# Kernel tuning notes

Measured on AMD Instinct MI355X. Metric: run time of the kernel, lower is better.

Reference implementation:

```python
import jax, jax.numpy as jnp
import numpy as np

LAMB_LABELS = 1.0
LAMB_BBOXES = 5.0
LAMB_GENIOU = 2.0


def box_cxcywh_to_xyxy(x):
    cx, cy, w, h = x[..., 0], x[..., 1], x[..., 2], x[..., 3]
    return jnp.stack([cx - 0.5 * w, cy - 0.5 * h, cx + 0.5 * w, cy + 0.5 * h], axis=-1)


def generalized_box_iou(b1, b2):
    # b1: [P,4] xyxy, b2: [T,4] xyxy -> [P,T] pairwise GIoU
    area1 = (b1[:, 2] - b1[:, 0]) * (b1[:, 3] - b1[:, 1])
    area2 = (b2[:, 2] - b2[:, 0]) * (b2[:, 3] - b2[:, 1])
    lt = jnp.maximum(b1[:, None, :2], b2[None, :, :2])
    rb = jnp.minimum(b1[:, None, 2:], b2[None, :, 2:])
    wh = jnp.clip(rb - lt, 0.0)
    inter = wh[..., 0] * wh[..., 1]
    union = area1[:, None] + area2[None, :] - inter
    iou = inter / union
    lt_e = jnp.minimum(b1[:, None, :2], b2[None, :, :2])
    rb_e = jnp.maximum(b1[:, None, 2:], b2[None, :, 2:])
    wh_e = jnp.clip(rb_e - lt_e, 0.0)
    area_e = wh_e[..., 0] * wh_e[..., 1]
    return iou - (area_e - union) / area_e


def setup_inputs() -> dict:
    key = jax.random.key(0)
    k1, k2, k3, k4 = jax.random.split(key, 4)
    B, N, C, T = 16, 900, 92, 960
    out_labels = jax.random.normal(k1, (B, N, C), dtype=jnp.float32)
    out_bboxes = jax.random.uniform(k2, (B, N, 4), dtype=jnp.float32)
    tgt_labels = jax.random.randint(k3, (T,), 0, C, dtype=jnp.int64)
    tgt_bboxes = jax.random.uniform(k4, (T, 4), dtype=jnp.float32)
    return {"out_labels": out_labels, "out_bboxes": out_bboxes,
            "tgt_labels": tgt_labels, "tgt_bboxes": tgt_bboxes}


def reference(out_labels, out_bboxes, tgt_labels, tgt_bboxes):
    B, N, C = out_labels.shape
    # '(b n) d' softmax over classes, then gather target-label columns
    probs = jax.nn.softmax(out_labels.reshape(B * N, C), axis=-1)
    cost_labels = 1.0 - probs[:, tgt_labels]                     # [BN, T]
    ob = out_bboxes.reshape(B * N, 4)
    # pairwise L1 (torch.cdist p=1)
    cost_bboxes = jnp.sum(jnp.abs(ob[:, None, :] - tgt_bboxes[None, :, :]), axis=-1)
    # NOTE: original converts only predicted boxes to xyxy (targets used as-is)
    cost_geniou = 1.0 - generalized_box_iou(box_cxcywh_to_xyxy(ob), tgt_bboxes)
    cost = (LAMB_LABELS * cost_labels + LAMB_BBOXES * cost_bboxes
            + LAMB_GENIOU * cost_geniou)
    return cost.reshape(B, N, -1)                                # [B, N, T]
```

## Files before the change

### kernel.cpp

```cpp
#include <hip/hip_runtime.h>
#include <math.h>

constexpr int kC = 92, kT = 960;
constexpr int kBN = 14400;
constexpr int WPB = 4;
constexpr int THREADS = WPB * 64;

typedef float vf2 __attribute__((ext_vector_type(2)));

__global__ __launch_bounds__(THREADS, 8) void matcher_kernel(
    const float* __restrict__ out_labels,
    const float* __restrict__ out_bboxes,
    const int*   __restrict__ tgt_labels,
    const float* __restrict__ tgt_bboxes,
    float*       __restrict__ cost)
{
    __shared__ float2 s_cl2[WPB][96];

    const int tid  = threadIdx.x;
    const int w    = tid >> 6;
    const int lane = tid & 63;
    const int p0   = (blockIdx.x * WPB + w) * 2;

    const float* lr0 = out_labels + (size_t)p0 * kC;
    const float* lr1 = lr0 + kC;
    float e00 = __expf(lr0[lane]);
    float e10 = __expf(lr1[lane]);
    float e01 = (lane + 64 < kC) ? __expf(lr0[lane + 64]) : 0.0f;
    float e11 = (lane + 64 < kC) ? __expf(lr1[lane + 64]) : 0.0f;
    float s0 = e00 + e01, s1 = e10 + e11;
    #pragma unroll
    for (int m = 1; m < 64; m <<= 1) {
        s0 += __shfl_xor(s0, m, 64);
        s1 += __shfl_xor(s1, m, 64);
    }
    float inv0 = __builtin_amdgcn_rcpf(s0);
    float inv1 = __builtin_amdgcn_rcpf(s1);
    s_cl2[w][lane] = make_float2(fmaf(-e00, inv0, 5.0f), fmaf(-e10, inv1, 5.0f));
    if (lane + 64 < kC)
        s_cl2[w][lane + 64] =
            make_float2(fmaf(-e01, inv0, 5.0f), fmaf(-e11, inv1, 5.0f));

    float4 bbA = ((const float4*)out_bboxes)[p0];
    float4 bbB = ((const float4*)out_bboxes)[p0 + 1];
    vf2 bcA = {bbA.x, bbA.y}, whA = {bbA.z, bbA.w};
    vf2 bcB = {bbB.x, bbB.y}, whB = {bbB.z, bbB.w};
    vf2 hA = whA * 0.5f,  hB = whB * 0.5f;
    vf2 b0A = bcA - hA,   b1A = bcA + hA;
    vf2 b0B = bcB - hB,   b1B = bcB + hB;
    float area1A = (b1A.x - b0A.x) * (b1A.y - b0A.y);
    float area1B = (b1B.x - b0B.x) * (b1B.y - b0B.y);

    asm volatile("s_waitcnt lgkmcnt(0)" ::: "memory");

    const float4* tb4 = (const float4*)tgt_bboxes;
    float* crow0 = cost + (size_t)p0 * kT;
    float* crow1 = crow0 + kT;

    auto row_cost = [&](vf2 b0, vf2 b1, vf2 bc, vf2 wh, float area1,
                        vf2 t0, vf2 t1, vf2 wt, float a2, float cls) -> float {
        vf2 lt = {fmaxf(b0.x, t0.x), fmaxf(b0.y, t0.y)};
        vf2 rb = {fminf(b1.x, t1.x), fminf(b1.y, t1.y)};
        vf2 iwu = rb - lt;
        float iw = fmaxf(iwu.x, 0.0f), ih = fmaxf(iwu.y, 0.0f);
        float inter = iw * ih;
        vf2 ew = (wh + wt) - iwu;
        float area_e = ew.x * ew.y;
        float uni = (area1 + a2) - inter;
        vf2 d0 = bc - t0, d1 = wh - t1;
        float l1 = fabsf(d0.x) + fabsf(d0.y) + fabsf(d1.x) + fabsf(d1.y);
        float num = fmaf(uni, uni, inter * area_e);
        float rcp = __builtin_amdgcn_rcpf(uni * area_e);
        float v = fmaf(5.0f, l1, cls);
        return fmaf(-2.0f * num, rcp, v);
    };

    #pragma unroll 5
    for (int k = 0; k < 15; ++k) {
        const int t = lane + 64 * k;
        float4 tbb = tb4[t];
        int    lb  = tgt_labels[t];
        float2 cls = s_cl2[w][lb];
        vf2 t0 = {tbb.x, tbb.y}, t1 = {tbb.z, tbb.w};
        vf2 wt = t1 - t0;
        float a2 = wt.x * wt.y;
        crow0[t] = row_cost(b0A, b1A, bcA, whA, area1A, t0, t1, wt, a2, cls.x);
        crow1[t] = row_cost(b0B, b1B, bcB, whB, area1B, t0, t1, wt, a2, cls.y);
    }
}

extern "C" void kernel_launch(void* const* d_in, const int* in_sizes, int n_in,
                              void* d_out, int out_size, void* d_ws, size_t ws_size,
                              hipStream_t stream) {
    const float* out_labels = (const float*)d_in[0];
    const float* out_bboxes = (const float*)d_in[1];
    const int*   tgt_labels = (const int*)d_in[2];
    const float* tgt_bboxes = (const float*)d_in[3];
    float* cost = (float*)d_out;
    dim3 grid(kBN / (WPB * 2));
    matcher_kernel<<<grid, THREADS, 0, stream>>>(out_labels, out_bboxes,
                                                 tgt_labels, tgt_bboxes, cost);
}
```

Before: 88.65 us.

## Process four prediction rows per wave and two targets per lane with vectorized stores

Each wave now handles four prediction rows instead of two, so every target box and label load is reused across four rows, and the class-cost table is stored as a float4 per class. Each lane processes two adjacent targets per iteration and writes float2 stores, with a 64-target tail loop. The grid halves, launch bounds drop to 4 blocks per CU, and register pressure rises. The kernel is dominated by output writes, so the gain is limited to fewer loads and wider stores.

After: 88.39 us, median of 2. Within noise of the previous version (-0.3%).

```diff
diff --git a/kernel.cpp b/kernel.cpp
--- a/kernel.cpp
+++ b/kernel.cpp
@@ -5,69 +5,68 @@
 constexpr int kBN = 14400;
 constexpr int WPB = 4;
 constexpr int THREADS = WPB * 64;
+constexpr int RPW = 4;
 
 typedef float vf2 __attribute__((ext_vector_type(2)));
 
-__global__ __launch_bounds__(THREADS, 8) void matcher_kernel(
+__global__ __launch_bounds__(THREADS, 4) void matcher_kernel(
     const float* __restrict__ out_labels,
     const float* __restrict__ out_bboxes,
     const int*   __restrict__ tgt_labels,
     const float* __restrict__ tgt_bboxes,
     float*       __restrict__ cost)
 {
-    __shared__ float2 s_cl2[WPB][96];
+    __shared__ float s_cl[WPB][96][4];
 
     const int tid  = threadIdx.x;
     const int w    = tid >> 6;
     const int lane = tid & 63;
-    const int p0   = (blockIdx.x * WPB + w) * 2;
+    const int p0   = (blockIdx.x * WPB + w) * RPW;
 
-    const float* lr0 = out_labels + (size_t)p0 * kC;
-    const float* lr1 = lr0 + kC;
-    float e00 = __expf(lr0[lane]);
-    float e10 = __expf(lr1[lane]);
-    float e01 = (lane + 64 < kC) ? __expf(lr0[lane + 64]) : 0.0f;
-    float e11 = (lane + 64 < kC) ? __expf(lr1[lane + 64]) : 0.0f;
-    float s0 = e00 + e01, s1 = e10 + e11;
+    const float* lr = out_labels + (size_t)p0 * kC;
+    float e0[RPW], e1[RPW], s[RPW];
+    #pragma unroll
+    for (int r = 0; r < RPW; ++r) {
+        e0[r] = __expf(lr[r * kC + lane]);
+        e1[r] = (lane + 64 < kC) ? __expf(lr[r * kC + lane + 64]) : 0.0f;
+        s[r] = e0[r] + e1[r];
+    }
     #pragma unroll
     for (int m = 1; m < 64; m <<= 1) {
-        s0 += __shfl_xor(s0, m, 64);
-        s1 += __shfl_xor(s1, m, 64);
+        #pragma unroll
+        for (int r = 0; r < RPW; ++r)
+            s[r] += __shfl_xor(s[r], m, 64);
     }
-    float inv0 = __builtin_amdgcn_rcpf(s0);
-    float inv1 = __builtin_amdgcn_rcpf(s1);
-    s_cl2[w][lane] = make_float2(fmaf(-e00, inv0, 5.0f), fmaf(-e10, inv1, 5.0f));
-    if (lane + 64 < kC)
-        s_cl2[w][lane + 64] =
-            make_float2(fmaf(-e01, inv0, 5.0f), fmaf(-e11, inv1, 5.0f));
+    #pragma unroll
+    for (int r = 0; r < RPW; ++r) {
+        float inv = __builtin_amdgcn_rcpf(s[r]);
+        s_cl[w][lane][r] = fmaf(-e0[r], inv, 5.0f);
+        if (lane + 64 < kC) s_cl[w][lane + 64][r] = fmaf(-e1[r], inv, 5.0f);
+    }
 
-    float4 bbA = ((const float4*)out_bboxes)[p0];
-    float4 bbB = ((const float4*)out_bboxes)[p0 + 1];
-    vf2 bcA = {bbA.x, bbA.y}, whA = {bbA.z, bbA.w};
-    vf2 bcB = {bbB.x, bbB.y}, whB = {bbB.z, bbB.w};
-    vf2 hA = whA * 0.5f,  hB = whB * 0.5f;
-    vf2 b0A = bcA - hA,   b1A = bcA + hA;
-    vf2 b0B = bcB - hB,   b1B = bcB + hB;
-    float area1A = (b1A.x - b0A.x) * (b1A.y - b0A.y);
-    float area1B = (b1B.x - b0B.x) * (b1B.y - b0B.y);
+    vf2 bc[RPW], wh[RPW], b0[RPW], b1[RPW]; float area1[RPW];
+    #pragma unroll
+    for (int r = 0; r < RPW; ++r) {
+        float4 bb = ((const float4*)out_bboxes)[p0 + r];
+        bc[r] = vf2{bb.x, bb.y}; wh[r] = vf2{bb.z, bb.w};
+        vf2 h = wh[r] * 0.5f;
+        b0[r] = bc[r] - h; b1[r] = bc[r] + h;
+        area1[r] = (b1[r].x - b0[r].x) * (b1[r].y - b0[r].y);
+    }
 
     asm volatile("s_waitcnt lgkmcnt(0)" ::: "memory");
 
-    const float4* tb4 = (const float4*)tgt_bboxes;
-    float* crow0 = cost + (size_t)p0 * kT;
-    float* crow1 = crow0 + kT;
-
-    auto row_cost = [&](vf2 b0, vf2 b1, vf2 bc, vf2 wh, float area1,
-                        vf2 t0, vf2 t1, vf2 wt, float a2, float cls) -> float {
-        vf2 lt = {fmaxf(b0.x, t0.x), fmaxf(b0.y, t0.y)};
-        vf2 rb = {fminf(b1.x, t1.x), fminf(b1.y, t1.y)};
+    auto row_cost = [&](int r, vf2 t0, vf2 t1, vf2 wt, float a2,
+                        float cls) -> float {
+        vf2 lt = {fmaxf(b0[r].x, t0.x), fmaxf(b0[r].y, t0.y)};
+        vf2 rb = {fminf(b1[r].x, t1.x), fminf(b1[r].y, t1.y)};
         vf2 iwu = rb - lt;
         float iw = fmaxf(iwu.x, 0.0f), ih = fmaxf(iwu.y, 0.0f);
         float inter = iw * ih;
-        vf2 ew = (wh + wt) - iwu;
+        vf2 ew = (wh[r] + wt) - iwu;
         float area_e = ew.x * ew.y;
-        float uni = (area1 + a2) - inter;
-        vf2 d0 = bc - t0, d1 = wh - t1;
+        float uni = (area1[r] + a2) - inter;
+        vf2 d0 = bc[r] - t0, d1 = wh[r] - t1;
         float l1 = fabsf(d0.x) + fabsf(d0.y) + fabsf(d1.x) + fabsf(d1.y);
         float num = fmaf(uni, uni, inter * area_e);
         float rcp = __builtin_amdgcn_rcpf(uni * area_e);
@@ -75,17 +74,43 @@
         return fmaf(-2.0f * num, rcp, v);
     };
 
-    #pragma unroll 5
-    for (int k = 0; k < 15; ++k) {
-        const int t = lane + 64 * k;
-        float4 tbb = tb4[t];
-        int    lb  = tgt_labels[t];
-        float2 cls = s_cl2[w][lb];
-        vf2 t0 = {tbb.x, tbb.y}, t1 = {tbb.z, tbb.w};
-        vf2 wt = t1 - t0;
-        float a2 = wt.x * wt.y;
-        crow0[t] = row_cost(b0A, b1A, bcA, whA, area1A, t0, t1, wt, a2, cls.x);
-        crow1[t] = row_cost(b0B, b1B, bcB, whB, area1B, t0, t1, wt, a2, cls.y);
+    const float4* tb4 = (const float4*)tgt_bboxes;
+    float* crow = cost + (size_t)p0 * kT;
+
+    #pragma unroll 2
+    for (int k = 0; k < 7; ++k) {
+        const int tA = lane * 2 + 128 * k;
+        float4 fa = tb4[tA];
+        float4 fb = tb4[tA + 1];
+        int2 lb = ((const int2*)tgt_labels)[lane + 64 * k];
+        float4 clsA = *(const float4*)s_cl[w][lb.x];
+        float4 clsB = *(const float4*)s_cl[w][lb.y];
+        vf2 ta0 = {fa.x, fa.y}, ta1 = {fa.z, fa.w};
+        vf2 tb0 = {fb.x, fb.y}, tb1 = {fb.z, fb.w};
+        vf2 wtA = ta1 - ta0, wtB = tb1 - tb0;
+        float a2A = wtA.x * wtA.y, a2B = wtB.x * wtB.y;
+        const float cA[4] = {clsA.x, clsA.y, clsA.z, clsA.w};
+        const float cB[4] = {clsB.x, clsB.y, clsB.z, clsB.w};
+        #pragma unroll
+        for (int r = 0; r < RPW; ++r) {
+            vf2 out;
+            out[0] = row_cost(r, ta0, ta1, wtA, a2A, cA[r]);
+            out[1] = row_cost(r, tb0, tb1, wtB, a2B, cB[r]);
+            *(vf2*)(crow + r * kT + tA) = out;
+        }
+    }
+
+    {
+        const int t = 896 + lane;
+        float4 ft = tb4[t];
+        int lb = tgt_labels[t];
+        float4 cls = *(const float4*)s_cl[w][lb];
+        vf2 t0 = {ft.x, ft.y}, t1 = {ft.z, ft.w};
+        vf2 wt = t1 - t0; float a2 = wt.x * wt.y;
+        const float cc[4] = {cls.x, cls.y, cls.z, cls.w};
+        #pragma unroll
+        for (int r = 0; r < RPW; ++r)
+            crow[r * kT + t] = row_cost(r, t0, t1, wt, a2, cc[r]);
     }
 }
 
@@ -97,7 +122,7 @@
     const int*   tgt_labels = (const int*)d_in[2];
     const float* tgt_bboxes = (const float*)d_in[3];
     float* cost = (float*)d_out;
-    dim3 grid(kBN / (WPB * 2));
+    dim3 grid(kBN / (WPB * RPW));
     matcher_kernel<<<grid, THREADS, 0, stream>>>(out_labels, out_bboxes,
                                                  tgt_labels, tgt_bboxes, cost);
 }
```
